# Performance work log

Hardware: AMD Instinct MI355X
Metric: run time of the kernel (lower is better)

Reference implementation:

```python
import jax, jax.numpy as jnp
import numpy as np

N_NODES = 50000
N_EDGES = 800000
IN_FEATS = 64
HIDDEN = 64
NUM_CLASSES = 32


def _graph_conv(x, src, dst, W, b, n_nodes):
    # DGL GraphConv, norm='both', allow_zero_in_degree=True:
    # out = D_in^{-1/2} * (A^T @ (D_out^{-1/2} * x)) @ W + b, degrees clamped to >=1
    e = src.shape[0]
    ones = jnp.ones((e,), dtype=x.dtype)
    out_deg = jax.ops.segment_sum(ones, src, num_segments=n_nodes)
    in_deg = jax.ops.segment_sum(ones, dst, num_segments=n_nodes)
    norm_src = jax.lax.rsqrt(jnp.maximum(out_deg, 1.0))[:, None]
    norm_dst = jax.lax.rsqrt(jnp.maximum(in_deg, 1.0))[:, None]
    h = x * norm_src                                   # [N, d]
    agg = jax.ops.segment_sum(h[src], dst, num_segments=n_nodes)  # gather+scatter over edges
    return (agg * norm_dst) @ W + b


def setup_inputs() -> dict:
    key = jax.random.key(0)
    k1, k2, k3, k4, k5 = jax.random.split(key, 5)
    features = jax.random.normal(k1, (N_NODES, IN_FEATS), dtype=jnp.float32)
    src = jax.random.randint(k2, (N_EDGES,), 0, N_NODES, dtype=jnp.int32)
    dst = jax.random.randint(k3, (N_EDGES,), 0, N_NODES, dtype=jnp.int32)
    W1 = jax.random.normal(k4, (IN_FEATS, HIDDEN), dtype=jnp.float32) * (1.0 / np.sqrt(IN_FEATS))
    b1 = jnp.zeros((HIDDEN,), dtype=jnp.float32)
    W2 = jax.random.normal(k5, (HIDDEN, NUM_CLASSES), dtype=jnp.float32) * (1.0 / np.sqrt(HIDDEN))
    b2 = jnp.zeros((NUM_CLASSES,), dtype=jnp.float32)
    return {"features": features, "src": src, "dst": dst,
            "W1": W1, "b1": b1, "W2": W2, "b2": b2}


def reference(features, src, dst, W1, b1, W2, b2) -> jnp.ndarray:
    n = features.shape[0]
    h = jax.nn.relu(_graph_conv(features, src, dst, W1, b1, n))
    out = _graph_conv(h, src, dst, W2, b2, n)
    # single canonical etype -> mean over one-element stack is identity
    return out
```

## Files before the change

kernel.cpp:

```cpp
#include <hip/hip_runtime.h>
#include <hip/hip_bf16.h>

#define N_NODES 50000
#define N_EDGES 800000
#define F 64
#define C 32
#define CAP 48

#define NPB   200
#define EPB   4000
#define NBUCK 196

static __device__ __forceinline__ float bf2f(unsigned short u) {
    return __uint_as_float(((unsigned)u) << 16);
}
static __device__ __forceinline__ unsigned short f2bf(float f) {
    __hip_bfloat16 h = __float2bfloat16(f);
    return *reinterpret_cast<unsigned short*>(&h);
}

__global__ void part_count_kernel(const int* __restrict__ src, const int* __restrict__ dst,
                                  int* __restrict__ bcnt_d, int* __restrict__ bcnt_s) {
    __shared__ int hd[NBUCK], hs[NBUCK];
    int t = threadIdx.x;
    for (int i = t; i < NBUCK; i += 256) { hd[i] = 0; hs[i] = 0; }
    __syncthreads();
    int b0 = blockIdx.x * EPB;
    for (int i = b0 + t; i < b0 + EPB; i += 256) {
        atomicAdd(&hd[dst[i] >> 8], 1);
        atomicAdd(&hs[src[i] >> 8], 1);
    }
    __syncthreads();
    for (int i = t; i < NBUCK; i += 256) {
        bcnt_d[blockIdx.x * NBUCK + i] = hd[i];
        bcnt_s[blockIdx.x * NBUCK + i] = hs[i];
    }
}

__global__ void part_scan_kernel(const int* __restrict__ bcnt_d, const int* __restrict__ bcnt_s,
                                 int* __restrict__ eoff_d, int* __restrict__ eoff_s,
                                 int* __restrict__ base_d, int* __restrict__ base_s) {
    __shared__ int tot_d[NBUCK], tot_s[NBUCK], bd[NBUCK + 1], bs[NBUCK + 1];
    int t = threadIdx.x;
    if (t < NBUCK) {
        int run = 0;
        for (int blk = 0; blk < NPB; blk++) {
            eoff_d[blk * NBUCK + t] = run;
            run += bcnt_d[blk * NBUCK + t];
        }
        tot_d[t] = run;
        run = 0;
        for (int blk = 0; blk < NPB; blk++) {
            eoff_s[blk * NBUCK + t] = run;
            run += bcnt_s[blk * NBUCK + t];
        }
        tot_s[t] = run;
    }
    __syncthreads();
    if (t == 0) {
        int r = 0;
        for (int b = 0; b < NBUCK; b++) { bd[b] = r; r += tot_d[b]; }
        bd[NBUCK] = r;
        r = 0;
        for (int b = 0; b < NBUCK; b++) { bs[b] = r; r += tot_s[b]; }
        bs[NBUCK] = r;
    }
    __syncthreads();
    if (t < NBUCK + 1) { base_d[t] = bd[t]; base_s[t] = bs[t]; }
}

__global__ void part_scatter_kernel(const int* __restrict__ src, const int* __restrict__ dst,
                                    const int* __restrict__ eoff_d, const int* __restrict__ eoff_s,
                                    const int* __restrict__ base_d, const int* __restrict__ base_s,
                                    int* __restrict__ edge_d, int* __restrict__ edge_s) {
    __shared__ int cd[NBUCK], cs[NBUCK];
    int t = threadIdx.x;
    for (int i = t; i < NBUCK; i += 256) {
        cd[i] = base_d[i] + eoff_d[blockIdx.x * NBUCK + i];
        cs[i] = base_s[i] + eoff_s[blockIdx.x * NBUCK + i];
    }
    __syncthreads();
    int b0 = blockIdx.x * EPB;
    for (int i = b0 + t; i < b0 + EPB; i += 256) {
        int d = dst[i], s = src[i];
        int p = atomicAdd(&cd[d >> 8], 1);
        edge_d[p] = ((d & 255) << 16) | s;
        int q = atomicAdd(&cs[s >> 8], 1);
        edge_s[q] = s & 255;
    }
}

__global__ void bucket_build_kernel(const int* __restrict__ edge_d, const int* __restrict__ edge_s,
                                    const int* __restrict__ base_d, const int* __restrict__ base_s,
                                    int* __restrict__ csr, int* __restrict__ cnt,
                                    float* __restrict__ norm_dst, float* __restrict__ norm_src) {
    __shared__ int cur[256];
    __shared__ int hs[256];
    int t = threadIdx.x;
    int bucket = blockIdx.x;
    cur[t] = 0;
    hs[t] = 0;
    __syncthreads();
    int lo = base_d[bucket], hi = base_d[bucket + 1];
    for (int i = lo + t; i < hi; i += 256) {
        int pd = edge_d[i];
        int dlow = pd >> 16;
        int s = pd & 0xFFFF;
        int pos = atomicAdd(&cur[dlow], 1);
        if (pos < CAP) csr[(size_t)(bucket * 256 + dlow) * CAP + pos] = s;
    }
    int slo = base_s[bucket], shi = base_s[bucket + 1];
    for (int i = slo + t; i < shi; i += 256) {
        atomicAdd(&hs[edge_s[i]], 1);
    }
    __syncthreads();
    int node = bucket * 256 + t;
    if (node < N_NODES) {
        int c = cur[t] < CAP ? cur[t] : CAP;
        cnt[node] = c;
        norm_dst[node] = rsqrtf(fmaxf((float)c, 1.0f));
        norm_src[node] = rsqrtf(fmaxf((float)hs[t], 1.0f));
    }
}

__global__ void gemm_y_kernel(const float* __restrict__ x,
                              const float* __restrict__ ns,
                              const float* __restrict__ W,
                              __hip_bfloat16* __restrict__ y) {
    __shared__ float sW[F * F];
    __shared__ float srow[16][F];
    int t = threadIdx.x;
    for (int i = t; i < F * F; i += 256) sW[i] = W[i];
    int j = t & 63;
    int w = t >> 6;
    int base = blockIdx.x * 16;
    for (int r = w; r < 16; r += 4) srow[r][j] = x[(size_t)(base + r) * F + j];
    __syncthreads();
    float a0 = 0, a1 = 0, a2 = 0, a3 = 0;
#pragma unroll
    for (int k = 0; k < F; k++) {
        float wv = sW[k * F + j];
        a0 += srow[w * 4 + 0][k] * wv;
        a1 += srow[w * 4 + 1][k] * wv;
        a2 += srow[w * 4 + 2][k] * wv;
        a3 += srow[w * 4 + 3][k] * wv;
    }
    int n0 = base + w * 4;
    y[(size_t)(n0 + 0) * F + j] = __float2bfloat16(a0 * ns[n0 + 0]);
    y[(size_t)(n0 + 1) * F + j] = __float2bfloat16(a1 * ns[n0 + 1]);
    y[(size_t)(n0 + 2) * F + j] = __float2bfloat16(a2 * ns[n0 + 2]);
    y[(size_t)(n0 + 3) * F + j] = __float2bfloat16(a3 * ns[n0 + 3]);
}

struct f4 { float x, y, z, w; };

static __device__ __forceinline__ void gacc(const __hip_bfloat16* __restrict__ tab,
                                            int s, int fo, f4& a) {
    const ushort4 v = *reinterpret_cast<const ushort4*>(
        reinterpret_cast<const unsigned short*>(tab) + (size_t)s * F + fo);
    a.x += bf2f(v.x); a.y += bf2f(v.y); a.z += bf2f(v.z); a.w += bf2f(v.w);
}

__global__ void gather64_kernel(const __hip_bfloat16* __restrict__ y,
                                const int* __restrict__ csr,
                                const int* __restrict__ cnt,
                                const float* __restrict__ norm_dst,
                                const float* __restrict__ norm_src,
                                const float* __restrict__ b1,
                                __hip_bfloat16* __restrict__ h2) {
    int gid  = blockIdx.x * blockDim.x + threadIdx.x;
    int node = gid >> 6;
    int lane = threadIdx.x & 63;
    if (node >= N_NODES) return;
    int g  = lane >> 4;
    int fo = (lane & 15) * 4;
    int n = cnt[node];
    const int* row = csr + (size_t)node * CAP;
    f4 a = {0.f, 0.f, 0.f, 0.f};
    int e = 0;
    for (; e + 15 < n; e += 16) {
        int4 idx = *reinterpret_cast<const int4*>(row + e + 4 * g);
        gacc(y, idx.x, fo, a);
        gacc(y, idx.y, fo, a);
        gacc(y, idx.z, fo, a);
        gacc(y, idx.w, fo, a);
    }
    for (; e < n; e += 4) {
        int ee = e + g;
        if (ee < n) gacc(y, row[ee], fo, a);
    }
    a.x += __shfl_down(a.x, 16); a.y += __shfl_down(a.y, 16);
    a.z += __shfl_down(a.z, 16); a.w += __shfl_down(a.w, 16);
    a.x += __shfl_down(a.x, 32); a.y += __shfl_down(a.y, 32);
    a.z += __shfl_down(a.z, 32); a.w += __shfl_down(a.w, 32);
    if (lane < 16) {
        float nd = norm_dst[node], ns = norm_src[node];
        ushort4 o;
        o.x = f2bf(fmaxf(a.x * nd + b1[fo + 0], 0.0f) * ns);
        o.y = f2bf(fmaxf(a.y * nd + b1[fo + 1], 0.0f) * ns);
        o.z = f2bf(fmaxf(a.z * nd + b1[fo + 2], 0.0f) * ns);
        o.w = f2bf(fmaxf(a.w * nd + b1[fo + 3], 0.0f) * ns);
        *reinterpret_cast<ushort4*>(
            reinterpret_cast<unsigned short*>(h2) + (size_t)node * F + fo) = o;
    }
}

__global__ void gather_gemm2_kernel(const __hip_bfloat16* __restrict__ h2,
                                    const int* __restrict__ csr,
                                    const int* __restrict__ cnt,
                                    const float* __restrict__ norm_dst,
                                    const float* __restrict__ W2,
                                    const float* __restrict__ b2,
                                    float* __restrict__ out) {
    __shared__ float sW[F * C];
    __shared__ float sagg[4][F];
    int t = threadIdx.x;
    for (int i = t; i < F * C; i += 256) sW[i] = W2[i];
    int w    = t >> 6;
    int lane = t & 63;
    int node = blockIdx.x * 4 + w;
    int g  = lane >> 4;
    int fo = (lane & 15) * 4;
    f4 a = {0.f, 0.f, 0.f, 0.f};
    if (node < N_NODES) {
        int n = cnt[node];
        const int* row = csr + (size_t)node * CAP;
        int e = 0;
        for (; e + 15 < n; e += 16) {
            int4 idx = *reinterpret_cast<const int4*>(row + e + 4 * g);
            gacc(h2, idx.x, fo, a);
            gacc(h2, idx.y, fo, a);
            gacc(h2, idx.z, fo, a);
            gacc(h2, idx.w, fo, a);
        }
        for (; e < n; e += 4) {
            int ee = e + g;
            if (ee < n) gacc(h2, row[ee], fo, a);
        }
    }
    a.x += __shfl_down(a.x, 16); a.y += __shfl_down(a.y, 16);
    a.z += __shfl_down(a.z, 16); a.w += __shfl_down(a.w, 16);
    a.x += __shfl_down(a.x, 32); a.y += __shfl_down(a.y, 32);
    a.z += __shfl_down(a.z, 32); a.w += __shfl_down(a.w, 32);
    if (lane < 16) {
        sagg[w][fo + 0] = a.x;
        sagg[w][fo + 1] = a.y;
        sagg[w][fo + 2] = a.z;
        sagg[w][fo + 3] = a.w;
    }
    __syncthreads();
    int j    = lane & 31;
    int half = lane >> 5;
    float o = 0.0f;
    if (node < N_NODES) {
#pragma unroll
        for (int k = 0; k < 32; k++) {
            int kk = half * 32 + k;
            o += sagg[w][kk] * sW[kk * C + j];
        }
    }
    o += __shfl_down(o, 32);
    if (node < N_NODES && half == 0)
        out[(size_t)node * C + j] = o * norm_dst[node] + b2[j];
}

extern "C" void kernel_launch(void* const* d_in, const int* in_sizes, int n_in,
                              void* d_out, int out_size, void* d_ws, size_t ws_size,
                              hipStream_t stream) {
    const float* features = (const float*)d_in[0];
    const int*   src      = (const int*)d_in[1];
    const int*   dst      = (const int*)d_in[2];
    const float* W1       = (const float*)d_in[3];
    const float* b1       = (const float*)d_in[4];
    const float* W2       = (const float*)d_in[5];
    const float* b2       = (const float*)d_in[6];
    float* out = (float*)d_out;

    char* p = (char*)d_ws;
    float* norm_src = (float*)p;  p += (size_t)N_NODES * 4;
    float* norm_dst = (float*)p;  p += (size_t)N_NODES * 4;
    int*   cnt      = (int*)p;    p += (size_t)N_NODES * 4;
    int*   csr      = (int*)p;    p += (size_t)N_NODES * CAP * 4;
    __hip_bfloat16* y  = (__hip_bfloat16*)p;  p += (size_t)N_NODES * F * 2;
    __hip_bfloat16* h2 = (__hip_bfloat16*)p;

    int* edge_d = (int*)y;
    int* edge_s = edge_d + N_EDGES;
    int* q = (int*)h2;
    int* bcnt_d = q;                 q += NPB * NBUCK;
    int* bcnt_s = q;                 q += NPB * NBUCK;
    int* eoff_d = q;                 q += NPB * NBUCK;
    int* eoff_s = q;                 q += NPB * NBUCK;
    int* base_d = q;                 q += NBUCK + 1;
    int* base_s = q;

    part_count_kernel<<<NPB, 256, 0, stream>>>(src, dst, bcnt_d, bcnt_s);
    part_scan_kernel<<<1, 256, 0, stream>>>(bcnt_d, bcnt_s, eoff_d, eoff_s, base_d, base_s);
    part_scatter_kernel<<<NPB, 256, 0, stream>>>(src, dst, eoff_d, eoff_s, base_d, base_s,
                                                 edge_d, edge_s);
    bucket_build_kernel<<<NBUCK, 256, 0, stream>>>(edge_d, edge_s, base_d, base_s,
                                                   csr, cnt, norm_dst, norm_src);

    gemm_y_kernel<<<N_NODES / 16, 256, 0, stream>>>(features, norm_src, W1, y);
    gather64_kernel<<<(N_NODES * 64) / 256, 256, 0, stream>>>(y, csr, cnt, norm_dst,
                                                              norm_src, b1, h2);

    gather_gemm2_kernel<<<(N_NODES + 3) / 4, 256, 0, stream>>>(h2, csr, cnt, norm_dst,
                                                               W2, b2, out);
}
```

Measured before the change: 210.0 us.

## Fuse CSR build kernels into one persistent kernel with grid barriers

The four graph-partition kernels (count, scan, scatter, bucket build) are merged into a single 200-block kernel whose phases are separated by a software grid barrier built on global atomics. The barrier counter is zeroed with a memset before launch. This removes three kernel launch gaps and the associated idle time. In exchange it relies on all 200 blocks being co-resident, which holds on this GPU's CU count, and it adds spin-wait barrier overhead plus a single-block scan phase while the other blocks wait.

```diff
diff --git a/kernel.cpp b/kernel.cpp
--- a/kernel.cpp
+++ b/kernel.cpp
@@ -19,107 +19,119 @@
     return *reinterpret_cast<unsigned short*>(&h);
 }
 
-__global__ void part_count_kernel(const int* __restrict__ src, const int* __restrict__ dst,
-                                  int* __restrict__ bcnt_d, int* __restrict__ bcnt_s) {
-    __shared__ int hd[NBUCK], hs[NBUCK];
+static __device__ __forceinline__ void grid_barrier(int* __restrict__ bar, int phase) {
+    __syncthreads();
+    if (threadIdx.x == 0) {
+        __threadfence();
+        int old = atomicAdd(&bar[0], 1);
+        if (old == NPB * phase - 1) {
+            atomicExch(&bar[16], phase);
+        } else {
+            while (atomicAdd(&bar[16], 0) < phase)
+                __builtin_amdgcn_s_sleep(8);
+        }
+        __threadfence();
+    }
+    __syncthreads();
+}
+
+__global__ void build_fused_kernel(const int* __restrict__ src, const int* __restrict__ dst,
+                                   int* __restrict__ bar,
+                                   int* __restrict__ bcnt_d, int* __restrict__ bcnt_s,
+                                   int* __restrict__ eoff_d, int* __restrict__ eoff_s,
+                                   int* __restrict__ base_d, int* __restrict__ base_s,
+                                   int* __restrict__ edge_d, int* __restrict__ edge_s,
+                                   int* __restrict__ csr, int* __restrict__ cnt,
+                                   float* __restrict__ norm_dst, float* __restrict__ norm_src) {
+    __shared__ int sh_hd[NBUCK], sh_hs[NBUCK];
+    __shared__ int sh_td[NBUCK], sh_ts[NBUCK];
+    __shared__ int sh_bd[NBUCK + 1], sh_bs[NBUCK + 1];
+    __shared__ int sh_cd[NBUCK], sh_cs[NBUCK];
+    __shared__ int sh_cur[256], sh_hn[256];
     int t = threadIdx.x;
-    for (int i = t; i < NBUCK; i += 256) { hd[i] = 0; hs[i] = 0; }
-    __syncthreads();
-    int b0 = blockIdx.x * EPB;
+    int b = blockIdx.x;
+
+    for (int i = t; i < NBUCK; i += 256) { sh_hd[i] = 0; sh_hs[i] = 0; }
+    __syncthreads();
+    int b0 = b * EPB;
     for (int i = b0 + t; i < b0 + EPB; i += 256) {
-        atomicAdd(&hd[dst[i] >> 8], 1);
-        atomicAdd(&hs[src[i] >> 8], 1);
+        atomicAdd(&sh_hd[dst[i] >> 8], 1);
+        atomicAdd(&sh_hs[src[i] >> 8], 1);
     }
     __syncthreads();
     for (int i = t; i < NBUCK; i += 256) {
-        bcnt_d[blockIdx.x * NBUCK + i] = hd[i];
-        bcnt_s[blockIdx.x * NBUCK + i] = hs[i];
-    }
-}
-
-__global__ void part_scan_kernel(const int* __restrict__ bcnt_d, const int* __restrict__ bcnt_s,
-                                 int* __restrict__ eoff_d, int* __restrict__ eoff_s,
-                                 int* __restrict__ base_d, int* __restrict__ base_s) {
-    __shared__ int tot_d[NBUCK], tot_s[NBUCK], bd[NBUCK + 1], bs[NBUCK + 1];
-    int t = threadIdx.x;
-    if (t < NBUCK) {
-        int run = 0;
-        for (int blk = 0; blk < NPB; blk++) {
-            eoff_d[blk * NBUCK + t] = run;
-            run += bcnt_d[blk * NBUCK + t];
-        }
-        tot_d[t] = run;
-        run = 0;
-        for (int blk = 0; blk < NPB; blk++) {
-            eoff_s[blk * NBUCK + t] = run;
-            run += bcnt_s[blk * NBUCK + t];
-        }
-        tot_s[t] = run;
-    }
-    __syncthreads();
-    if (t == 0) {
-        int r = 0;
-        for (int b = 0; b < NBUCK; b++) { bd[b] = r; r += tot_d[b]; }
-        bd[NBUCK] = r;
-        r = 0;
-        for (int b = 0; b < NBUCK; b++) { bs[b] = r; r += tot_s[b]; }
-        bs[NBUCK] = r;
-    }
-    __syncthreads();
-    if (t < NBUCK + 1) { base_d[t] = bd[t]; base_s[t] = bs[t]; }
-}
-
-__global__ void part_scatter_kernel(const int* __restrict__ src, const int* __restrict__ dst,
-                                    const int* __restrict__ eoff_d, const int* __restrict__ eoff_s,
-                                    const int* __restrict__ base_d, const int* __restrict__ base_s,
-                                    int* __restrict__ edge_d, int* __restrict__ edge_s) {
-    __shared__ int cd[NBUCK], cs[NBUCK];
-    int t = threadIdx.x;
+        bcnt_d[b * NBUCK + i] = sh_hd[i];
+        bcnt_s[b * NBUCK + i] = sh_hs[i];
+    }
+    grid_barrier(bar, 1);
+
+    if (b == 0) {
+        if (t < NBUCK) {
+            int run = 0;
+            for (int blk = 0; blk < NPB; blk++) {
+                eoff_d[blk * NBUCK + t] = run;
+                run += bcnt_d[blk * NBUCK + t];
+            }
+            sh_td[t] = run;
+            run = 0;
+            for (int blk = 0; blk < NPB; blk++) {
+                eoff_s[blk * NBUCK + t] = run;
+                run += bcnt_s[blk * NBUCK + t];
+            }
+            sh_ts[t] = run;
+        }
+        __syncthreads();
+        if (t == 0) {
+            int r = 0;
+            for (int k = 0; k < NBUCK; k++) { sh_bd[k] = r; r += sh_td[k]; }
+            sh_bd[NBUCK] = r;
+            r = 0;
+            for (int k = 0; k < NBUCK; k++) { sh_bs[k] = r; r += sh_ts[k]; }
+            sh_bs[NBUCK] = r;
+        }
+        __syncthreads();
+        if (t < NBUCK + 1) { base_d[t] = sh_bd[t]; base_s[t] = sh_bs[t]; }
+    }
+    grid_barrier(bar, 2);
+
     for (int i = t; i < NBUCK; i += 256) {
-        cd[i] = base_d[i] + eoff_d[blockIdx.x * NBUCK + i];
-        cs[i] = base_s[i] + eoff_s[blockIdx.x * NBUCK + i];
-    }
-    __syncthreads();
-    int b0 = blockIdx.x * EPB;
+        sh_cd[i] = base_d[i] + eoff_d[b * NBUCK + i];
+        sh_cs[i] = base_s[i] + eoff_s[b * NBUCK + i];
+    }
+    __syncthreads();
     for (int i = b0 + t; i < b0 + EPB; i += 256) {
         int d = dst[i], s = src[i];
-        int p = atomicAdd(&cd[d >> 8], 1);
+        int p = atomicAdd(&sh_cd[d >> 8], 1);
         edge_d[p] = ((d & 255) << 16) | s;
-        int q = atomicAdd(&cs[s >> 8], 1);
+        int q = atomicAdd(&sh_cs[s >> 8], 1);
         edge_s[q] = s & 255;
     }
-}
-
-__global__ void bucket_build_kernel(const int* __restrict__ edge_d, const int* __restrict__ edge_s,
-                                    const int* __restrict__ base_d, const int* __restrict__ base_s,
-                                    int* __restrict__ csr, int* __restrict__ cnt,
-                                    float* __restrict__ norm_dst, float* __restrict__ norm_src) {
-    __shared__ int cur[256];
-    __shared__ int hs[256];
-    int t = threadIdx.x;
-    int bucket = blockIdx.x;
-    cur[t] = 0;
-    hs[t] = 0;
-    __syncthreads();
-    int lo = base_d[bucket], hi = base_d[bucket + 1];
-    for (int i = lo + t; i < hi; i += 256) {
-        int pd = edge_d[i];
-        int dlow = pd >> 16;
-        int s = pd & 0xFFFF;
-        int pos = atomicAdd(&cur[dlow], 1);
-        if (pos < CAP) csr[(size_t)(bucket * 256 + dlow) * CAP + pos] = s;
-    }
-    int slo = base_s[bucket], shi = base_s[bucket + 1];
-    for (int i = slo + t; i < shi; i += 256) {
-        atomicAdd(&hs[edge_s[i]], 1);
-    }
-    __syncthreads();
-    int node = bucket * 256 + t;
-    if (node < N_NODES) {
-        int c = cur[t] < CAP ? cur[t] : CAP;
-        cnt[node] = c;
-        norm_dst[node] = rsqrtf(fmaxf((float)c, 1.0f));
-        norm_src[node] = rsqrtf(fmaxf((float)hs[t], 1.0f));
+    grid_barrier(bar, 3);
+
+    if (b < NBUCK) {
+        sh_cur[t] = 0;
+        sh_hn[t] = 0;
+        __syncthreads();
+        int lo = base_d[b], hi = base_d[b + 1];
+        for (int i = lo + t; i < hi; i += 256) {
+            int pd = edge_d[i];
+            int dlow = pd >> 16;
+            int s = pd & 0xFFFF;
+            int pos = atomicAdd(&sh_cur[dlow], 1);
+            if (pos < CAP) csr[(size_t)(b * 256 + dlow) * CAP + pos] = s;
+        }
+        int slo = base_s[b], shi = base_s[b + 1];
+        for (int i = slo + t; i < shi; i += 256) {
+            atomicAdd(&sh_hn[edge_s[i]], 1);
+        }
+        __syncthreads();
+        int node = b * 256 + t;
+        if (node < N_NODES) {
+            int c = sh_cur[t] < CAP ? sh_cur[t] : CAP;
+            cnt[node] = c;
+            norm_dst[node] = rsqrtf(fmaxf((float)c, 1.0f));
+            norm_src[node] = rsqrtf(fmaxf((float)sh_hn[t], 1.0f));
+        }
     }
 }
 
@@ -277,6 +289,7 @@
     float* out = (float*)d_out;
 
     char* p = (char*)d_ws;
+    int*   bar      = (int*)p;    p += 128;
     float* norm_src = (float*)p;  p += (size_t)N_NODES * 4;
     float* norm_dst = (float*)p;  p += (size_t)N_NODES * 4;
     int*   cnt      = (int*)p;    p += (size_t)N_NODES * 4;
@@ -294,12 +307,11 @@
     int* base_d = q;                 q += NBUCK + 1;
     int* base_s = q;
 
-    part_count_kernel<<<NPB, 256, 0, stream>>>(src, dst, bcnt_d, bcnt_s);
-    part_scan_kernel<<<1, 256, 0, stream>>>(bcnt_d, bcnt_s, eoff_d, eoff_s, base_d, base_s);
-    part_scatter_kernel<<<NPB, 256, 0, stream>>>(src, dst, eoff_d, eoff_s, base_d, base_s,
-                                                 edge_d, edge_s);
-    bucket_build_kernel<<<NBUCK, 256, 0, stream>>>(edge_d, edge_s, base_d, base_s,
-                                                   csr, cnt, norm_dst, norm_src);
+    hipMemsetAsync(bar, 0, 128, stream);
+    build_fused_kernel<<<NPB, 256, 0, stream>>>(src, dst, bar,
+                                                bcnt_d, bcnt_s, eoff_d, eoff_s,
+                                                base_d, base_s, edge_d, edge_s,
+                                                csr, cnt, norm_dst, norm_src);
 
     gemm_y_kernel<<<N_NODES / 16, 256, 0, stream>>>(features, norm_src, W1, y);
     gather64_kernel<<<(N_NODES * 64) / 256, 256, 0, stream>>>(y, csr, cnt, norm_dst,
```

Result: slower. 255.0 us (+21.4%).
